# Optimization experiments

Hardware: AMD Instinct MI355X
Metric: run time of the kernel (lower is better)

Reference implementation:

```python
import jax, jax.numpy as jnp
import numpy as np

N = 50000   # nodes per graph stream
E = 800000  # edges per graph stream
G = 100     # graphs in batch
FIN, H = 74, 256


def setup_inputs() -> dict:
    key = jax.random.key(0)
    ks = jax.random.split(key, 16)
    d = {
        'xl': jax.random.normal(ks[0], (N, FIN), jnp.float32),
        'xr': jax.random.normal(ks[1], (N, FIN), jnp.float32),
        'src_l': jax.random.randint(ks[2], (E,), 0, N, jnp.int32),
        'dst_l': jax.random.randint(ks[3], (E,), 0, N, jnp.int32),
        'src_r': jax.random.randint(ks[4], (E,), 0, N, jnp.int32),
        'dst_r': jax.random.randint(ks[5], (E,), 0, N, jnp.int32),
        'gid_l': jnp.sort(jax.random.randint(ks[6], (N,), 0, G, jnp.int32)),
        'gid_r': jnp.sort(jax.random.randint(ks[7], (N,), 0, G, jnp.int32)),
        'W0': jax.random.normal(ks[8], (FIN, H), jnp.float32) / np.sqrt(FIN),
        'b0': jnp.zeros((H,), jnp.float32),
        'W1': jax.random.normal(ks[9], (H, H), jnp.float32) / np.sqrt(H),
        'b1': jnp.zeros((H,), jnp.float32),
        'W2': jax.random.normal(ks[10], (H, H), jnp.float32) / np.sqrt(H),
        'b2': jnp.zeros((H,), jnp.float32),
        'Wf1': jax.random.normal(ks[11], (2 * H, H), jnp.float32) / np.sqrt(2 * H),
        'bf1': jnp.zeros((H,), jnp.float32),
        'Wf2': jax.random.normal(ks[12], (H, 1), jnp.float32) / np.sqrt(H),
        'bf2': jnp.zeros((1,), jnp.float32),
    }
    return d


def _deg_isqrt(idx, n):
    deg = jax.ops.segment_sum(jnp.ones_like(idx, jnp.float32), idx, num_segments=n)
    return jax.lax.rsqrt(jnp.maximum(deg, 1.0))


def _graph_conv(x, src, dst, do_isq, di_isq, W, b):
    # DGL GraphConv, norm='both': h = relu(D_in^{-1/2} A D_out^{-1/2} X W + b)
    h = (x * do_isq[:, None]) @ W            # transform-first (in_feats >= out for layer0 path is fine mathematically)
    agg = jax.ops.segment_sum(h[src], dst, num_segments=x.shape[0])
    return jax.nn.relu(agg * di_isq[:, None] + b)


def reference(xl, xr, src_l, dst_l, src_r, dst_r, gid_l, gid_r,
              W0, b0, W1, b1, W2, b2, Wf1, bf1, Wf2, bf2):
    do_l, di_l = _deg_isqrt(src_l, N), _deg_isqrt(dst_l, N)
    do_r, di_r = _deg_isqrt(src_r, N), _deg_isqrt(dst_r, N)
    Ws, bs = (W0, W1, W2), (b0, b1, b2)
    hl, hr = xl, xr
    for W, b in zip(Ws, bs):  # shared weights across both graph streams
        hl = _graph_conv(hl, src_l, dst_l, do_l, di_l, W, b)
        hr = _graph_conv(hr, src_r, dst_r, do_r, di_r, W, b)
    pl = jax.ops.segment_sum(hl, gid_l, num_segments=G)  # dgl.sum_nodes
    pr = jax.ops.segment_sum(hr, gid_r, num_segments=G)
    z = jnp.concatenate([pl, pr], axis=-1)               # [G, 2H]
    return jax.nn.relu(z @ Wf1 + bf1) @ Wf2 + bf2        # [G, 1]
```

## Files before the change

### kernel.cpp

```cpp
#include <hip/hip_runtime.h>

#define N_NODES 50000
#define N_EDGES 800000
#define N_GRAPHS 100
#define FIN_DIM 74
#define X_LD 80
#define K0PAD 96
#define H_DIM 256
#define EG 3125
#define XSCALE_BLKS 15625
#define AGG_BLOCKS 25000
#define GEMM_BLKS 782
#define POOL_BLKS 782
#define SCAN_BLOCKS 196

typedef float f32x4 __attribute__((ext_vector_type(4)));
typedef unsigned short us2 __attribute__((ext_vector_type(2)));
typedef unsigned short us4 __attribute__((ext_vector_type(4)));
typedef unsigned short us8 __attribute__((ext_vector_type(8)));
typedef __bf16 bf16x8 __attribute__((ext_vector_type(8)));

__device__ __forceinline__ unsigned short f2bf(float x) {
    unsigned u = __builtin_bit_cast(unsigned, x);
    u += 0x7fff + ((u >> 16) & 1);
    return (unsigned short)(u >> 16);
}
__device__ __forceinline__ float bf2f(unsigned short h) {
    return __builtin_bit_cast(float, (unsigned)h << 16);
}


__device__ __forceinline__ void hist_body(int bid, const int* __restrict__ src,
                                          const int* __restrict__ dst,
                                          int* __restrict__ cs, int* __restrict__ fc,
                                          int* __restrict__ rk) {
    int e = bid * 256 + threadIdx.x;
    if (e < N_EDGES) {
        rk[e] = atomicAdd(&fc[dst[e]], 1);
        atomicAdd(&cs[src[e]], 1);
    }
}

__device__ __forceinline__ void scat_body(int bid, const int* __restrict__ src,
                                          const int* __restrict__ dst,
                                          const int* __restrict__ rp,
                                          const int* __restrict__ rk,
                                          int* __restrict__ col) {
    int e = bid * 256 + threadIdx.x;
    if (e < N_EDGES) {
        int d = dst[e];
        col[rp[d] + rk[e]] = src[e];
    }
}

__device__ __forceinline__ void xscale_body(int bid, const float* __restrict__ x,
                                            const float* __restrict__ dso,
                                            unsigned short* __restrict__ xp) {
    int id = bid * 256 + threadIdx.x;
    int n = id / X_LD, f = id - n * X_LD;
    float v = (f < FIN_DIM) ? x[(size_t)n * FIN_DIM + f] * dso[n] : 0.f;
    xp[id] = f2bf(v);
}

template<int LDI, int LDO>
__device__ __forceinline__ void agg_body(int nb, const unsigned short* __restrict__ h,
                                         const int* __restrict__ rp,
                                         const int* __restrict__ col,
                                         unsigned short* __restrict__ A) {
    int n = nb * 2 + (threadIdx.x >> 7);
    int f2 = (threadIdx.x & 127) * 2;
    if (f2 >= LDI) {
        if (f2 < LDO) { us2 z = {0, 0}; *(us2*)&A[(size_t)n * LDO + f2] = z; }
        return;
    }
    int beg = rp[n], end = rp[n + 1];
    float a0 = 0.f, a1 = 0.f, b0 = 0.f, b1 = 0.f;
    int j = beg;
    for (; j + 3 < end; j += 4) {
        int s0 = col[j], s1 = col[j + 1], s2 = col[j + 2], s3 = col[j + 3];
        us2 v0 = *(const us2*)&h[(size_t)s0 * LDI + f2];
        us2 v1 = *(const us2*)&h[(size_t)s1 * LDI + f2];
        us2 v2 = *(const us2*)&h[(size_t)s2 * LDI + f2];
        us2 v3 = *(const us2*)&h[(size_t)s3 * LDI + f2];
        a0 += bf2f(v0[0]) + bf2f(v1[0]);
        a1 += bf2f(v0[1]) + bf2f(v1[1]);
        b0 += bf2f(v2[0]) + bf2f(v3[0]);
        b1 += bf2f(v2[1]) + bf2f(v3[1]);
    }
    for (; j < end; ++j) {
        int s = col[j];
        us2 v = *(const us2*)&h[(size_t)s * LDI + f2];
        a0 += bf2f(v[0]);
        a1 += bf2f(v[1]);
    }
    us2 r = { f2bf(a0 + b0), f2bf(a1 + b1) };
    *(us2*)&A[(size_t)n * LDO + f2] = r;
}

__device__ __forceinline__ void pool_body(int nb, const unsigned short* __restrict__ h,
                                          const int* __restrict__ gid,
                                          float* __restrict__ pool) {
    int n0 = nb * 64;
    int f = threadIdx.x;
    int end = min(n0 + 64, N_NODES);
    float acc = 0.0f;
    int gcur = gid[n0];
    for (int i = n0; i < end; ++i) {
        int g = gid[i];
        if (g != gcur) {
            atomicAdd(&pool[(size_t)gcur * H_DIM + f], acc);
            acc = 0.0f;
            gcur = g;
        }
        acc += bf2f(h[(size_t)i * H_DIM + f]);
    }
    atomicAdd(&pool[(size_t)gcur * H_DIM + f], acc);
}

template<int K, int KW>
__device__ __forceinline__ void gemm_body(int id, const unsigned short* __restrict__ A,
                                          const float* __restrict__ W,
                                          const float* __restrict__ bias,
                                          const float* __restrict__ dsi,
                                          const float* __restrict__ scale,
                                          unsigned short* __restrict__ C,
                                          unsigned short* smem) {
    unsigned short (*Ah)[40] = (unsigned short(*)[40])smem;
    unsigned short (*Bh)[36] = (unsigned short(*)[36])(smem + 128 * 40);
    const int M = N_NODES;

    int tid = threadIdx.x;
    int lane = tid & 63, wid = tid >> 6;
    int wm = (wid >> 1) * 64, wn = (wid & 1) * 64;
    int bm = (id >> 1) * 128, bn = (id & 1) * 128;

    f32x4 acc[4][4] = {};
    int r0 = wm + (lane & 15);
    int c0 = wn + (lane & 15);
    int kA = (lane >> 4) * 8;

    for (int k0 = 0; k0 < K; k0 += 32) {
        #pragma unroll
        for (int i = 0; i < 2; ++i) {
            int q = tid + i * 256;
            int row = q >> 2, k8 = (q & 3) * 8;
            int gm = bm + row;
            us8 v = {0, 0, 0, 0, 0, 0, 0, 0};
            if (gm < M) v = *(const us8*)(A + (size_t)gm * K + k0 + k8);
            *(us8*)&Ah[row][k8] = v;
        }
        {
            int colx = tid & 127, kg = tid >> 7;
            #pragma unroll
            for (int g = 0; g < 4; ++g) {
                us4 hh;
                #pragma unroll
                for (int j = 0; j < 4; ++j) {
                    int gk = k0 + kg * 16 + g * 4 + j;
                    float w = (gk < KW) ? W[(size_t)gk * H_DIM + bn + colx] : 0.f;
                    hh[j] = f2bf(w);
                }
                *(us4*)&Bh[colx][kg * 16 + g * 4] = hh;
            }
        }
        __syncthreads();

        bf16x8 ah[4], bh[4];
        #pragma unroll
        for (int m = 0; m < 4; ++m)
            ah[m] = __builtin_bit_cast(bf16x8, *(const us8*)&Ah[r0 + m * 16][kA]);
        #pragma unroll
        for (int n = 0; n < 4; ++n) {
            us4 x0 = *(const us4*)&Bh[c0 + n * 16][kA];
            us4 x1 = *(const us4*)&Bh[c0 + n * 16][kA + 4];
            us8 x;
            x[0] = x0[0]; x[1] = x0[1]; x[2] = x0[2]; x[3] = x0[3];
            x[4] = x1[0]; x[5] = x1[1]; x[6] = x1[2]; x[7] = x1[3];
            bh[n] = __builtin_bit_cast(bf16x8, x);
        }

        #pragma unroll
        for (int m = 0; m < 4; ++m)
            #pragma unroll
            for (int n = 0; n < 4; ++n)
                acc[m][n] = __builtin_amdgcn_mfma_f32_16x16x32_bf16(ah[m], bh[n], acc[m][n], 0, 0, 0);
        __syncthreads();
    }

    int rowq = (lane >> 4) * 4;
    #pragma unroll
    for (int n = 0; n < 4; ++n) {
        int gn = bn + wn + n * 16 + (lane & 15);
        float bv = bias[gn];
        #pragma unroll
        for (int m = 0; m < 4; ++m) {
            #pragma unroll
            for (int j = 0; j < 4; ++j) {
                int gm = bm + wm + m * 16 + rowq + j;
                if (gm < M) {
                    float r = fmaxf(acc[m][n][j] * dsi[gm] + bv, 0.0f);
                    if (scale) r *= scale[gm];
                    C[(size_t)gm * H_DIM + gn] = f2bf(r);
                }
            }
        }
    }
}


__device__ __forceinline__ int block_excl_scan(int v, int* wsums) {
    int lane = threadIdx.x & 63, w = threadIdx.x >> 6;
    int x = v;
    #pragma unroll
    for (int ofs = 1; ofs < 64; ofs <<= 1) {
        int y = __shfl_up(x, ofs, 64);
        if (lane >= ofs) x += y;
    }
    if (lane == 63) wsums[w] = x;
    __syncthreads();
    int wo = 0;
    #pragma unroll
    for (int k = 0; k < 4; ++k) if (k < w) wo += wsums[k];
    return wo + x - v;
}

__global__ void hist_kernel(const int* __restrict__ src, const int* __restrict__ dst,
                            int* __restrict__ cs, int* __restrict__ fc, int* __restrict__ rk) {
    hist_body(blockIdx.x, src, dst, cs, fc, rk);
}

__global__ void deg_scan1_kernel(const int* __restrict__ cs, const int* __restrict__ fc,
                                 float* __restrict__ dso, float* __restrict__ dsi,
                                 int* __restrict__ rp, int* __restrict__ bs) {
    __shared__ int ws[4];
    int i = blockIdx.x * 256 + threadIdx.x;
    int v = 0;
    if (i < N_NODES) {
        dso[i] = rsqrtf(fmaxf((float)cs[i], 1.0f));
        v = fc[i];
        dsi[i] = rsqrtf(fmaxf((float)v, 1.0f));
    }
    int ex = block_excl_scan(v, ws);
    if (i < N_NODES) rp[i] = ex;
    if (threadIdx.x == 255) bs[blockIdx.x] = ex + v;
}

__global__ void scan2_kernel(int* __restrict__ bs, int nb) {
    __shared__ int ws[4];
    int i = threadIdx.x;
    int v = (i < nb) ? bs[i] : 0;
    int ex = block_excl_scan(v, ws);
    __syncthreads();
    if (i < nb) bs[i] = ex;
}

__global__ void scan3_kernel(int* __restrict__ rp, const int* __restrict__ bs) {
    int i = blockIdx.x * 256 + threadIdx.x;
    if (i < N_NODES) rp[i] += bs[blockIdx.x];
    if (i == 0) rp[N_NODES] = N_EDGES;
}

__global__ void fuse_hsx(const int* __restrict__ srcR, const int* __restrict__ dstR,
                         int* __restrict__ csR, int* __restrict__ fcR, int* __restrict__ rkR,
                         const int* __restrict__ srcL, const int* __restrict__ dstL,
                         const int* __restrict__ rpL, const int* __restrict__ rkL,
                         int* __restrict__ colL,
                         const float* __restrict__ xL, const float* __restrict__ dsoL,
                         unsigned short* __restrict__ xpL) {
    int bid = blockIdx.x;
    if (bid < EG)            hist_body(bid, srcR, dstR, csR, fcR, rkR);
    else if (bid < 2 * EG)   scat_body(bid - EG, srcL, dstL, rpL, rkL, colL);
    else                     xscale_body(bid - 2 * EG, xL, dsoL, xpL);
}

__global__ void fuse_dsagg0(const int* __restrict__ csR, const int* __restrict__ fcR,
                            float* __restrict__ dsoR, float* __restrict__ dsiR,
                            int* __restrict__ rpR, int* __restrict__ bsR,
                            const unsigned short* __restrict__ xpL, const int* __restrict__ rpL,
                            const int* __restrict__ colL, unsigned short* __restrict__ AL) {
    __shared__ int ws[4];
    int bid = blockIdx.x;
    if (bid < SCAN_BLOCKS) {
        int i = bid * 256 + threadIdx.x;
        int v = 0;
        if (i < N_NODES) {
            dsoR[i] = rsqrtf(fmaxf((float)csR[i], 1.0f));
            v = fcR[i];
            dsiR[i] = rsqrtf(fmaxf((float)v, 1.0f));
        }
        int ex = block_excl_scan(v, ws);
        if (i < N_NODES) rpR[i] = ex;
        if (threadIdx.x == 255) bsR[bid] = ex + v;
    } else {
        agg_body<X_LD, K0PAD>(bid - SCAN_BLOCKS, xpL, rpL, colL, AL);
    }
}

__global__ void fuse_sxagg(const int* __restrict__ srcR, const int* __restrict__ dstR,
                           const int* __restrict__ rpR, const int* __restrict__ rkR,
                           int* __restrict__ colR,
                           const float* __restrict__ xR, const float* __restrict__ dsoR,
                           unsigned short* __restrict__ xpR,
                           const unsigned short* __restrict__ hL, const int* __restrict__ rpL,
                           const int* __restrict__ colL, unsigned short* __restrict__ AL) {
    int bid = blockIdx.x;
    if (bid < EG)                      scat_body(bid, srcR, dstR, rpR, rkR, colR);
    else if (bid < EG + XSCALE_BLKS)   xscale_body(bid - EG, xR, dsoR, xpR);
    else                               agg_body<H_DIM, H_DIM>(bid - EG - XSCALE_BLKS, hL, rpL, colL, AL);
}

__global__ void fuse_agg_agg(const unsigned short* __restrict__ hL, const int* __restrict__ rpL,
                             const int* __restrict__ colL, unsigned short* __restrict__ AL,
                             const unsigned short* __restrict__ xpR, const int* __restrict__ rpR,
                             const int* __restrict__ colR, unsigned short* __restrict__ AR) {
    int bid = blockIdx.x;
    if (bid & 1) agg_body<X_LD, K0PAD>(bid >> 1, xpR, rpR, colR, AR);
    else         agg_body<H_DIM, H_DIM>(bid >> 1, hL, rpL, colL, AL);
}

__global__ void fuse_pool_agg(const unsigned short* __restrict__ hP, const int* __restrict__ gidP,
                              float* __restrict__ poolP,
                              const unsigned short* __restrict__ hA, const int* __restrict__ rpA,
                              const int* __restrict__ colA, unsigned short* __restrict__ outA) {
    int bid = blockIdx.x;
    if (bid < POOL_BLKS) pool_body(bid, hP, gidP, poolP);
    else                 agg_body<H_DIM, H_DIM>(bid - POOL_BLKS, hA, rpA, colA, outA);
}

template<int K, int KW>
__global__ __launch_bounds__(256) void gemm_kernel(
        const unsigned short* __restrict__ A, const float* __restrict__ W,
        const float* __restrict__ bias, const float* __restrict__ dsi,
        const float* __restrict__ scale, unsigned short* __restrict__ C) {
    __shared__ unsigned short smem[128 * 40 + 128 * 36];
    gemm_body<K, KW>(blockIdx.x, A, W, bias, dsi, scale, C, smem);
}

__global__ __launch_bounds__(256) void gemm_pair_kernel(
        const unsigned short* __restrict__ A1, const float* __restrict__ Wa,
        const float* __restrict__ ba, const float* __restrict__ dsi1, unsigned short* __restrict__ C1,
        const unsigned short* __restrict__ A2, const float* __restrict__ Wb,
        const float* __restrict__ bb, const float* __restrict__ dsi2,
        const float* __restrict__ sc2, unsigned short* __restrict__ C2) {
    __shared__ unsigned short smem[128 * 40 + 128 * 36];
    int bid = blockIdx.x;
    if (bid < GEMM_BLKS) gemm_body<H_DIM, H_DIM>(bid, A1, Wa, ba, dsi1, nullptr, C1, smem);
    else                 gemm_body<K0PAD, FIN_DIM>(bid - GEMM_BLKS, A2, Wb, bb, dsi2, sc2, C2, smem);
}

__global__ void agg_kernel(const unsigned short* __restrict__ h, const int* __restrict__ rp,
                           const int* __restrict__ col, unsigned short* __restrict__ A) {
    agg_body<H_DIM, H_DIM>(blockIdx.x, h, rp, col, A);
}

__global__ void pool_kernel(const unsigned short* __restrict__ h, const int* __restrict__ gid,
                            float* __restrict__ pool) {
    pool_body(blockIdx.x, h, gid, pool);
}

__global__ __launch_bounds__(256) void mlp_kernel(
        const float* __restrict__ pl, const float* __restrict__ pr,
        const float* __restrict__ Wf1, const float* __restrict__ bf1,
        const float* __restrict__ Wf2, const float* __restrict__ bf2,
        float* __restrict__ out) {
    __shared__ float z[512];
    __shared__ float red[256];
    int g = blockIdx.x, tid = threadIdx.x;
    z[tid] = pl[(size_t)g * H_DIM + tid];
    z[tid + 256] = pr[(size_t)g * H_DIM + tid];
    __syncthreads();
    float t = bf1[tid];
    #pragma unroll 8
    for (int k = 0; k < 512; ++k) t += z[k] * Wf1[(size_t)k * H_DIM + tid];
    t = fmaxf(t, 0.0f);
    red[tid] = t * Wf2[tid];
    __syncthreads();
    for (int ofs = 128; ofs > 0; ofs >>= 1) {
        if (tid < ofs) red[tid] += red[tid + ofs];
        __syncthreads();
    }
    if (tid == 0) out[g] = red[0] + bf2[0];
}


extern "C" void kernel_launch(void* const* d_in, const int* in_sizes, int n_in,
                              void* d_out, int out_size, void* d_ws, size_t ws_size,
                              hipStream_t stream) {
    const float* xl   = (const float*)d_in[0];
    const float* xr   = (const float*)d_in[1];
    const int* src_l  = (const int*)d_in[2];
    const int* dst_l  = (const int*)d_in[3];
    const int* src_r  = (const int*)d_in[4];
    const int* dst_r  = (const int*)d_in[5];
    const int* gid_l  = (const int*)d_in[6];
    const int* gid_r  = (const int*)d_in[7];
    const float* W0   = (const float*)d_in[8];
    const float* b0   = (const float*)d_in[9];
    const float* W1   = (const float*)d_in[10];
    const float* b1   = (const float*)d_in[11];
    const float* W2   = (const float*)d_in[12];
    const float* b2   = (const float*)d_in[13];
    const float* Wf1  = (const float*)d_in[14];
    const float* bf1  = (const float*)d_in[15];
    const float* Wf2  = (const float*)d_in[16];
    const float* bf2  = (const float*)d_in[17];
    float* out = (float*)d_out;
    (void)in_sizes; (void)n_in; (void)out_size; (void)ws_size;

    size_t off = 0;
    auto carve = [&](size_t bytes) {
        void* p = (char*)d_ws + off;
        off += (bytes + 255) & ~(size_t)255;
        return p;
    };
    const size_t NB4 = (size_t)N_NODES * 4;

    char* zstart = (char*)d_ws;
    int*   cs_l   = (int*)carve(NB4);
    int*   fc_l   = (int*)carve(NB4);
    int*   cs_r   = (int*)carve(NB4);
    int*   fc_r   = (int*)carve(NB4);
    float* pool_l = (float*)carve((size_t)N_GRAPHS * H_DIM * 4);
    float* pool_r = (float*)carve((size_t)N_GRAPHS * H_DIM * 4);
    size_t zbytes = off;

    float* dso_l = (float*)carve(NB4);
    float* dsi_l = (float*)carve(NB4);
    float* dso_r = (float*)carve(NB4);
    float* dsi_r = (float*)carve(NB4);
    int*   rp_l  = (int*)carve((size_t)(N_NODES + 1) * 4);
    int*   rp_r  = (int*)carve((size_t)(N_NODES + 1) * 4);
    int*   col_l = (int*)carve((size_t)N_EDGES * 4);
    int*   col_r = (int*)carve((size_t)N_EDGES * 4);
    int*   rk_l  = (int*)carve((size_t)N_EDGES * 4);
    int*   rk_r  = (int*)carve((size_t)N_EDGES * 4);
    int*   bs_l  = (int*)carve((size_t)SCAN_BLOCKS * 4);
    int*   bs_r  = (int*)carve((size_t)SCAN_BLOCKS * 4);

    unsigned short* xp_l  = (unsigned short*)carve((size_t)N_NODES * X_LD * 2);
    unsigned short* xp_r  = (unsigned short*)carve((size_t)N_NODES * X_LD * 2);
    unsigned short* bufA_l = (unsigned short*)carve((size_t)N_NODES * H_DIM * 2);
    unsigned short* bufA_r = (unsigned short*)carve((size_t)N_NODES * H_DIM * 2);
    unsigned short* bufH_l = (unsigned short*)carve((size_t)N_NODES * H_DIM * 2);
    unsigned short* bufH_r = (unsigned short*)carve((size_t)N_NODES * H_DIM * 2);

    hipMemsetAsync(zstart, 0, zbytes, stream);

    hist_kernel<<<EG, 256, 0, stream>>>(src_l, dst_l, cs_l, fc_l, rk_l);
    deg_scan1_kernel<<<SCAN_BLOCKS, 256, 0, stream>>>(cs_l, fc_l, dso_l, dsi_l, rp_l, bs_l);
    scan2_kernel<<<1, 256, 0, stream>>>(bs_l, SCAN_BLOCKS);
    scan3_kernel<<<SCAN_BLOCKS, 256, 0, stream>>>(rp_l, bs_l);

    fuse_hsx<<<2 * EG + XSCALE_BLKS, 256, 0, stream>>>(
        src_r, dst_r, cs_r, fc_r, rk_r,
        src_l, dst_l, rp_l, rk_l, col_l,
        xl, dso_l, xp_l);

    fuse_dsagg0<<<SCAN_BLOCKS + AGG_BLOCKS, 256, 0, stream>>>(
        cs_r, fc_r, dso_r, dsi_r, rp_r, bs_r,
        xp_l, rp_l, col_l, bufA_l);
    scan2_kernel<<<1, 256, 0, stream>>>(bs_r, SCAN_BLOCKS);
    scan3_kernel<<<SCAN_BLOCKS, 256, 0, stream>>>(rp_r, bs_r);

    gemm_kernel<K0PAD, FIN_DIM><<<GEMM_BLKS, 256, 0, stream>>>(bufA_l, W0, b0, dsi_l, dso_l, bufH_l);

    fuse_sxagg<<<EG + XSCALE_BLKS + AGG_BLOCKS, 256, 0, stream>>>(
        src_r, dst_r, rp_r, rk_r, col_r,
        xr, dso_r, xp_r,
        bufH_l, rp_l, col_l, bufA_l);

    gemm_kernel<H_DIM, H_DIM><<<GEMM_BLKS, 256, 0, stream>>>(bufA_l, W1, b1, dsi_l, dso_l, bufH_l);

    fuse_agg_agg<<<2 * AGG_BLOCKS, 256, 0, stream>>>(
        bufH_l, rp_l, col_l, bufA_l,
        xp_r, rp_r, col_r, bufA_r);

    gemm_pair_kernel<<<2 * GEMM_BLKS, 256, 0, stream>>>(
        bufA_l, W2, b2, dsi_l, bufH_l,
        bufA_r, W0, b0, dsi_r, dso_r, bufH_r);

    fuse_pool_agg<<<POOL_BLKS + AGG_BLOCKS, 256, 0, stream>>>(
        bufH_l, gid_l, pool_l,
        bufH_r, rp_r, col_r, bufA_r);

    gemm_kernel<H_DIM, H_DIM><<<GEMM_BLKS, 256, 0, stream>>>(bufA_r, W1, b1, dsi_r, dso_r, bufH_r);

    agg_kernel<<<AGG_BLOCKS, 256, 0, stream>>>(bufH_r, rp_r, col_r, bufA_r);
    gemm_kernel<H_DIM, H_DIM><<<GEMM_BLKS, 256, 0, stream>>>(bufA_r, W2, b2, dsi_r, nullptr, bufH_r);
    pool_kernel<<<POOL_BLKS, 256, 0, stream>>>(bufH_r, gid_r, pool_r);

    mlp_kernel<<<N_GRAPHS, 256, 0, stream>>>(pool_l, pool_r, Wf1, bf1, Wf2, bf2, out);
}
```

Before: 921.3 us.

## Slice node features into column panels and pre-convert weights to bf16

```diff
diff --git a/kernel.cpp b/kernel.cpp
--- a/kernel.cpp
+++ b/kernel.cpp
@@ -4,19 +4,19 @@
 #define N_EDGES 800000
 #define N_GRAPHS 100
 #define FIN_DIM 74
-#define X_LD 80
-#define K0PAD 96
+#define K0 96
 #define H_DIM 256
 #define EG 3125
-#define XSCALE_BLKS 15625
-#define AGG_BLOCKS 25000
+#define XS_BLKS 18750
+#define WCONV_BLKS 608
+#define AGG0_BLKS 3128
+#define AGGH_BLKS 6256
 #define GEMM_BLKS 782
 #define POOL_BLKS 782
 #define SCAN_BLOCKS 196
 
 typedef float f32x4 __attribute__((ext_vector_type(4)));
-typedef unsigned short us2 __attribute__((ext_vector_type(2)));
-typedef unsigned short us4 __attribute__((ext_vector_type(4)));
+typedef unsigned int u32x4 __attribute__((ext_vector_type(4)));
 typedef unsigned short us8 __attribute__((ext_vector_type(8)));
 typedef __bf16 bf16x8 __attribute__((ext_vector_type(8)));
 
@@ -27,6 +27,14 @@
 }
 __device__ __forceinline__ float bf2f(unsigned short h) {
     return __builtin_bit_cast(float, (unsigned)h << 16);
+}
+__device__ __forceinline__ void acc8(float* a, us8 v) {
+    u32x4 w = __builtin_bit_cast(u32x4, v);
+    #pragma unroll
+    for (int i = 0; i < 4; ++i) {
+        a[2 * i]     += __builtin_bit_cast(float, w[i] << 16);
+        a[2 * i + 1] += __builtin_bit_cast(float, w[i] & 0xffff0000u);
+    }
 }
 
 
@@ -57,44 +65,63 @@
                                             const float* __restrict__ dso,
                                             unsigned short* __restrict__ xp) {
     int id = bid * 256 + threadIdx.x;
-    int n = id / X_LD, f = id - n * X_LD;
+    int n = id / 96, f = id - n * 96;
     float v = (f < FIN_DIM) ? x[(size_t)n * FIN_DIM + f] * dso[n] : 0.f;
-    xp[id] = f2bf(v);
-}
-
-template<int LDI, int LDO>
-__device__ __forceinline__ void agg_body(int nb, const unsigned short* __restrict__ h,
+    xp[(size_t)(f >> 4) * (N_NODES * 16) + (size_t)n * 16 + (f & 15)] = f2bf(v);
+}
+
+__device__ __forceinline__ void wconv_body(int bid, const float* __restrict__ W0,
+                                           const float* __restrict__ W1,
+                                           const float* __restrict__ W2,
+                                           unsigned short* __restrict__ Wt) {
+    int id = bid * 256 + threadIdx.x;
+    if (id < 256 * 96) {
+        int n = id / 96, k = id - n * 96;
+        float v = (k < FIN_DIM) ? W0[(size_t)k * H_DIM + n] : 0.f;
+        Wt[id] = f2bf(v);
+    } else if (id < 256 * 96 + 65536) {
+        int id2 = id - 256 * 96;
+        int n = id2 >> 8, k = id2 & 255;
+        Wt[id] = f2bf(W1[(size_t)k * H_DIM + n]);
+    } else {
+        int id3 = id - 256 * 96 - 65536;
+        int n = id3 >> 8, k = id3 & 255;
+        Wt[id] = f2bf(W2[(size_t)k * H_DIM + n]);
+    }
+}
+
+template<int SW, int NACT, int NSL>
+__device__ __forceinline__ void agg_body(int abid, int cg,
+                                         const unsigned short* __restrict__ h,
                                          const int* __restrict__ rp,
                                          const int* __restrict__ col,
                                          unsigned short* __restrict__ A) {
-    int n = nb * 2 + (threadIdx.x >> 7);
-    int f2 = (threadIdx.x & 127) * 2;
-    if (f2 >= LDI) {
-        if (f2 < LDO) { us2 z = {0, 0}; *(us2*)&A[(size_t)n * LDO + f2] = z; }
-        return;
-    }
+    const int CPB = SW / 8;
+    const int NPB = 256 / CPB;
+    if (cg >= NSL) return;
+    int slot = threadIdx.x & (CPB - 1);
+    int n = (abid >> 3) * NPB + threadIdx.x / CPB;
+    if (n >= N_NODES) return;
+    unsigned short* dst = A + (size_t)cg * (N_NODES * SW) + (size_t)n * SW + slot * 8;
+    if (cg >= NACT) { us8 z = {}; *(us8*)dst = z; return; }
+    const unsigned short* hs = h + (size_t)cg * (N_NODES * SW) + slot * 8;
     int beg = rp[n], end = rp[n + 1];
-    float a0 = 0.f, a1 = 0.f, b0 = 0.f, b1 = 0.f;
+    float a[8] = {};
     int j = beg;
     for (; j + 3 < end; j += 4) {
         int s0 = col[j], s1 = col[j + 1], s2 = col[j + 2], s3 = col[j + 3];
-        us2 v0 = *(const us2*)&h[(size_t)s0 * LDI + f2];
-        us2 v1 = *(const us2*)&h[(size_t)s1 * LDI + f2];
-        us2 v2 = *(const us2*)&h[(size_t)s2 * LDI + f2];
-        us2 v3 = *(const us2*)&h[(size_t)s3 * LDI + f2];
-        a0 += bf2f(v0[0]) + bf2f(v1[0]);
-        a1 += bf2f(v0[1]) + bf2f(v1[1]);
-        b0 += bf2f(v2[0]) + bf2f(v3[0]);
-        b1 += bf2f(v2[1]) + bf2f(v3[1]);
-    }
-    for (; j < end; ++j) {
-        int s = col[j];
-        us2 v = *(const us2*)&h[(size_t)s * LDI + f2];
-        a0 += bf2f(v[0]);
-        a1 += bf2f(v[1]);
-    }
-    us2 r = { f2bf(a0 + b0), f2bf(a1 + b1) };
-    *(us2*)&A[(size_t)n * LDO + f2] = r;
+        us8 v0 = *(const us8*)(hs + (size_t)s0 * SW);
+        us8 v1 = *(const us8*)(hs + (size_t)s1 * SW);
+        us8 v2 = *(const us8*)(hs + (size_t)s2 * SW);
+        us8 v3 = *(const us8*)(hs + (size_t)s3 * SW);
+        acc8(a, v0); acc8(a, v1); acc8(a, v2); acc8(a, v3);
+    }
+    for (; j < end; ++j)
+        acc8(a, *(const us8*)(hs + (size_t)col[j] * SW));
+    us8 r;
+    #pragma unroll
+    for (int i = 0; i < 8; ++i) r[i] = f2bf(a[i]);
+    *(us8*)dst = r;
 }
 
 __device__ __forceinline__ void pool_body(int nb, const unsigned short* __restrict__ h,
@@ -102,6 +129,7 @@
                                           float* __restrict__ pool) {
     int n0 = nb * 64;
     int f = threadIdx.x;
+    const unsigned short* hf = h + (size_t)(f >> 5) * (N_NODES * 32) + (f & 31);
     int end = min(n0 + 64, N_NODES);
     float acc = 0.0f;
     int gcur = gid[n0];
@@ -112,21 +140,21 @@
             acc = 0.0f;
             gcur = g;
         }
-        acc += bf2f(h[(size_t)i * H_DIM + f]);
+        acc += bf2f(hf[(size_t)i * 32]);
     }
     atomicAdd(&pool[(size_t)gcur * H_DIM + f], acc);
 }
 
-template<int K, int KW>
+template<int K, int SW>
 __device__ __forceinline__ void gemm_body(int id, const unsigned short* __restrict__ A,
-                                          const float* __restrict__ W,
+                                          const unsigned short* __restrict__ Wt,
                                           const float* __restrict__ bias,
                                           const float* __restrict__ dsi,
                                           const float* __restrict__ scale,
                                           unsigned short* __restrict__ C,
                                           unsigned short* smem) {
     unsigned short (*Ah)[40] = (unsigned short(*)[40])smem;
-    unsigned short (*Bh)[36] = (unsigned short(*)[36])(smem + 128 * 40);
+    unsigned short (*Bh)[40] = (unsigned short(*)[40])(smem + 128 * 40);
     const int M = N_NODES;
 
     int tid = threadIdx.x;
@@ -145,23 +173,20 @@
             int q = tid + i * 256;
             int row = q >> 2, k8 = (q & 3) * 8;
             int gm = bm + row;
-            us8 v = {0, 0, 0, 0, 0, 0, 0, 0};
-            if (gm < M) v = *(const us8*)(A + (size_t)gm * K + k0 + k8);
+            int kk = k0 + k8;
+            us8 v = {};
+            if (gm < M)
+                v = *(const us8*)(A + (size_t)(kk / SW) * ((size_t)N_NODES * SW)
+                                    + (size_t)gm * SW + (kk % SW));
             *(us8*)&Ah[row][k8] = v;
         }
         {
             int colx = tid & 127, kg = tid >> 7;
-            #pragma unroll
-            for (int g = 0; g < 4; ++g) {
-                us4 hh;
-                #pragma unroll
-                for (int j = 0; j < 4; ++j) {
-                    int gk = k0 + kg * 16 + g * 4 + j;
-                    float w = (gk < KW) ? W[(size_t)gk * H_DIM + bn + colx] : 0.f;
-                    hh[j] = f2bf(w);
-                }
-                *(us4*)&Bh[colx][kg * 16 + g * 4] = hh;
-            }
+            const unsigned short* wsrc = Wt + (size_t)(bn + colx) * K + k0 + kg * 16;
+            us8 w0 = *(const us8*)(wsrc);
+            us8 w1 = *(const us8*)(wsrc + 8);
+            *(us8*)&Bh[colx][kg * 16] = w0;
+            *(us8*)&Bh[colx][kg * 16 + 8] = w1;
         }
         __syncthreads();
 
@@ -170,14 +195,8 @@
         for (int m = 0; m < 4; ++m)
             ah[m] = __builtin_bit_cast(bf16x8, *(const us8*)&Ah[r0 + m * 16][kA]);
         #pragma unroll
-        for (int n = 0; n < 4; ++n) {
-            us4 x0 = *(const us4*)&Bh[c0 + n * 16][kA];
-            us4 x1 = *(const us4*)&Bh[c0 + n * 16][kA + 4];
-            us8 x;
-            x[0] = x0[0]; x[1] = x0[1]; x[2] = x0[2]; x[3] = x0[3];
-            x[4] = x1[0]; x[5] = x1[1]; x[6] = x1[2]; x[7] = x1[3];
-            bh[n] = __builtin_bit_cast(bf16x8, x);
-        }
+        for (int n = 0; n < 4; ++n)
+            bh[n] = __builtin_bit_cast(bf16x8, *(const us8*)&Bh[c0 + n * 16][kA]);
 
         #pragma unroll
         for (int m = 0; m < 4; ++m)
@@ -192,6 +211,7 @@
     for (int n = 0; n < 4; ++n) {
         int gn = bn + wn + n * 16 + (lane & 15);
         float bv = bias[gn];
+        unsigned short* cs = C + (size_t)(gn >> 5) * (N_NODES * 32) + (gn & 31);
         #pragma unroll
         for (int m = 0; m < 4; ++m) {
             #pragma unroll
@@ -200,7 +220,7 @@
                 if (gm < M) {
                     float r = fmaxf(acc[m][n][j] * dsi[gm] + bv, 0.0f);
                     if (scale) r *= scale[gm];
-                    C[(size_t)gm * H_DIM + gn] = f2bf(r);
+                    cs[(size_t)gm * 32] = f2bf(r);
                 }
             }
         }
@@ -224,9 +244,13 @@
     return wo + x - v;
 }
 
-__global__ void hist_kernel(const int* __restrict__ src, const int* __restrict__ dst,
-                            int* __restrict__ cs, int* __restrict__ fc, int* __restrict__ rk) {
-    hist_body(blockIdx.x, src, dst, cs, fc, rk);
+__global__ void k_whist(const float* __restrict__ W0, const float* __restrict__ W1,
+                        const float* __restrict__ W2, unsigned short* __restrict__ Wt,
+                        const int* __restrict__ src, const int* __restrict__ dst,
+                        int* __restrict__ cs, int* __restrict__ fc, int* __restrict__ rk) {
+    int bid = blockIdx.x;
+    if (bid < WCONV_BLKS) wconv_body(bid, W0, W1, W2, Wt);
+    else                  hist_body(bid - WCONV_BLKS, src, dst, cs, fc, rk);
 }
 
 __global__ void deg_scan1_kernel(const int* __restrict__ cs, const int* __restrict__ fc,
@@ -292,7 +316,7 @@
         if (i < N_NODES) rpR[i] = ex;
         if (threadIdx.x == 255) bsR[bid] = ex + v;
     } else {
-        agg_body<X_LD, K0PAD>(bid - SCAN_BLOCKS, xpL, rpL, colL, AL);
+        agg_body<16, 5, 6>(bid - SCAN_BLOCKS, blockIdx.x & 7, xpL, rpL, colL, AL);
     }
 }
 
@@ -304,9 +328,9 @@
                            const unsigned short* __restrict__ hL, const int* __restrict__ rpL,
                            const int* __restrict__ colL, unsigned short* __restrict__ AL) {
     int bid = blockIdx.x;
-    if (bid < EG)                      scat_body(bid, srcR, dstR, rpR, rkR, colR);
-    else if (bid < EG + XSCALE_BLKS)   xscale_body(bid - EG, xR, dsoR, xpR);
-    else                               agg_body<H_DIM, H_DIM>(bid - EG - XSCALE_BLKS, hL, rpL, colL, AL);
+    if (bid < EG)                    scat_body(bid, srcR, dstR, rpR, rkR, colR);
+    else if (bid < EG + XS_BLKS)     xscale_body(bid - EG, xR, dsoR, xpR);
+    else agg_body<32, 8, 8>(bid - EG - XS_BLKS, blockIdx.x & 7, hL, rpL, colL, AL);
 }
 
 __global__ void fuse_agg_agg(const unsigned short* __restrict__ hL, const int* __restrict__ rpL,
@@ -314,8 +338,8 @@
                              const unsigned short* __restrict__ xpR, const int* __restrict__ rpR,
                              const int* __restrict__ colR, unsigned short* __restrict__ AR) {
     int bid = blockIdx.x;
-    if (bid & 1) agg_body<X_LD, K0PAD>(bid >> 1, xpR, rpR, colR, AR);
-    else         agg_body<H_DIM, H_DIM>(bid >> 1, hL, rpL, colL, AL);
+    if (bid < AGGH_BLKS) agg_body<32, 8, 8>(bid, blockIdx.x & 7, hL, rpL, colL, AL);
+    else agg_body<16, 5, 6>(bid - AGGH_BLKS, blockIdx.x & 7, xpR, rpR, colR, AR);
 }
 
 __global__ void fuse_pool_agg(const unsigned short* __restrict__ hP, const int* __restrict__ gidP,
@@ -324,33 +348,33 @@
                               const int* __restrict__ colA, unsigned short* __restrict__ outA) {
     int bid = blockIdx.x;
     if (bid < POOL_BLKS) pool_body(bid, hP, gidP, poolP);
-    else                 agg_body<H_DIM, H_DIM>(bid - POOL_BLKS, hA, rpA, colA, outA);
-}
-
-template<int K, int KW>
+    else agg_body<32, 8, 8>(bid - POOL_BLKS, blockIdx.x & 7, hA, rpA, colA, outA);
+}
+
+template<int K, int SW>
 __global__ __launch_bounds__(256) void gemm_kernel(
-        const unsigned short* __restrict__ A, const float* __restrict__ W,
+        const unsigned short* __restrict__ A, const unsigned short* __restrict__ Wt,
         const float* __restrict__ bias, const float* __restrict__ dsi,
         const float* __restrict__ scale, unsigned short* __restrict__ C) {
-    __shared__ unsigned short smem[128 * 40 + 128 * 36];
-    gemm_body<K, KW>(blockIdx.x, A, W, bias, dsi, scale, C, smem);
+    __shared__ unsigned short smem[2 * 128 * 40];
+    gemm_body<K, SW>(blockIdx.x, A, Wt, bias, dsi, scale, C, smem);
 }
 
 __global__ __launch_bounds__(256) void gemm_pair_kernel(
-        const unsigned short* __restrict__ A1, const float* __restrict__ Wa,
-        const float* __restrict__ ba, const float* __restrict__ dsi1, unsigned short* __restrict__ C1,
-        const unsigned short* __restrict__ A2, const float* __restrict__ Wb,
-        const float* __restrict__ bb, const float* __restrict__ dsi2,
+        const unsigned short* __restrict__ A1, const unsigned short* __restrict__ Wt2,
+        const float* __restrict__ b2_, const float* __restrict__ dsi1, unsigned short* __restrict__ C1,
+        const unsigned short* __restrict__ A2, const unsigned short* __restrict__ Wt0,
+        const float* __restrict__ b0_, const float* __restrict__ dsi2,
         const float* __restrict__ sc2, unsigned short* __restrict__ C2) {
-    __shared__ unsigned short smem[128 * 40 + 128 * 36];
-    int bid = blockIdx.x;
-    if (bid < GEMM_BLKS) gemm_body<H_DIM, H_DIM>(bid, A1, Wa, ba, dsi1, nullptr, C1, smem);
-    else                 gemm_body<K0PAD, FIN_DIM>(bid - GEMM_BLKS, A2, Wb, bb, dsi2, sc2, C2, smem);
+    __shared__ unsigned short smem[2 * 128 * 40];
+    int bid = blockIdx.x;
+    if (bid < GEMM_BLKS) gemm_body<H_DIM, 32>(bid, A1, Wt2, b2_, dsi1, nullptr, C1, smem);
+    else                 gemm_body<K0, 16>(bid - GEMM_BLKS, A2, Wt0, b0_, dsi2, sc2, C2, smem);
 }
 
 __global__ void agg_kernel(const unsigned short* __restrict__ h, const int* __restrict__ rp,
                            const int* __restrict__ col, unsigned short* __restrict__ A) {
-    agg_body<H_DIM, H_DIM>(blockIdx.x, h, rp, col, A);
+    agg_body<32, 8, 8>(blockIdx.x, blockIdx.x & 7, h, rp, col, A);
 }
 
 __global__ void pool_kernel(const unsigned short* __restrict__ h, const int* __restrict__ gid,
@@ -437,8 +461,12 @@
     int*   bs_l  = (int*)carve((size_t)SCAN_BLOCKS * 4);
     int*   bs_r  = (int*)carve((size_t)SCAN_BLOCKS * 4);
 
-    unsigned short* xp_l  = (unsigned short*)carve((size_t)N_NODES * X_LD * 2);
-    unsigned short* xp_r  = (unsigned short*)carve((size_t)N_NODES * X_LD * 2);
+    unsigned short* Wt    = (unsigned short*)carve((size_t)(256 * 96 + 2 * 65536) * 2);
+    unsigned short* Wt0   = Wt;
+    unsigned short* Wt1   = Wt + 256 * 96;
+    unsigned short* Wt2   = Wt + 256 * 96 + 65536;
+    unsigned short* xp_l  = (unsigned short*)carve((size_t)N_NODES * 96 * 2);
+    unsigned short* xp_r  = (unsigned short*)carve((size_t)N_NODES * 96 * 2);
     unsigned short* bufA_l = (unsigned short*)carve((size_t)N_NODES * H_DIM * 2);
     unsigned short* bufA_r = (unsigned short*)carve((size_t)N_NODES * H_DIM * 2);
     unsigned short* bufH_l = (unsigned short*)carve((size_t)N_NODES * H_DIM * 2);
@@ -446,47 +474,48 @@
 
     hipMemsetAsync(zstart, 0, zbytes, stream);
 
-    hist_kernel<<<EG, 256, 0, stream>>>(src_l, dst_l, cs_l, fc_l, rk_l);
+    k_whist<<<WCONV_BLKS + EG, 256, 0, stream>>>(W0, W1, W2, Wt,
+                                                 src_l, dst_l, cs_l, fc_l, rk_l);
     deg_scan1_kernel<<<SCAN_BLOCKS, 256, 0, stream>>>(cs_l, fc_l, dso_l, dsi_l, rp_l, bs_l);
     scan2_kernel<<<1, 256, 0, stream>>>(bs_l, SCAN_BLOCKS);
     scan3_kernel<<<SCAN_BLOCKS, 256, 0, stream>>>(rp_l, bs_l);
 
-    fuse_hsx<<<2 * EG + XSCALE_BLKS, 256, 0, stream>>>(
+    fuse_hsx<<<2 * EG + XS_BLKS, 256, 0, stream>>>(
         src_r, dst_r, cs_r, fc_r, rk_r,
         src_l, dst_l, rp_l, rk_l, col_l,
         xl, dso_l, xp_l);
 
-    fuse_dsagg0<<<SCAN_BLOCKS + AGG_BLOCKS, 256, 0, stream>>>(
+    fuse_dsagg0<<<SCAN_BLOCKS + AGG0_BLKS, 256, 0, stream>>>(
         cs_r, fc_r, dso_r, dsi_r, rp_r, bs_r,
         xp_l, rp_l, col_l, bufA_l);
     scan2_kernel<<<1, 256, 0, stream>>>(bs_r, SCAN_BLOCKS);
     scan3_kernel<<<SCAN_BLOCKS, 256, 0, stream>>>(rp_r, bs_r);
 
-    gemm_kernel<K0PAD, FIN_DIM><<<GEMM_BLKS, 256, 0, stream>>>(bufA_l, W0, b0, dsi_l, dso_l, bufH_l);
-
-    fuse_sxagg<<<EG + XSCALE_BLKS + AGG_BLOCKS, 256, 0, stream>>>(
+    gemm_kernel<K0, 16><<<GEMM_BLKS, 256, 0, stream>>>(bufA_l, Wt0, b0, dsi_l, dso_l, bufH_l);
+
+    fuse_sxagg<<<EG + XS_BLKS + AGGH_BLKS, 256, 0, stream>>>(
         src_r, dst_r, rp_r, rk_r, col_r,
         xr, dso_r, xp_r,
         bufH_l, rp_l, col_l, bufA_l);
 
-    gemm_kernel<H_DIM, H_DIM><<<GEMM_BLKS, 256, 0, stream>>>(bufA_l, W1, b1, dsi_l, dso_l, bufH_l);
-
-    fuse_agg_agg<<<2 * AGG_BLOCKS, 256, 0, stream>>>(
+    gemm_kernel<H_DIM, 32><<<GEMM_BLKS, 256, 0, stream>>>(bufA_l, Wt1, b1, dsi_l, dso_l, bufH_l);
+
+    fuse_agg_agg<<<AGGH_BLKS + AGG0_BLKS, 256, 0, stream>>>(
         bufH_l, rp_l, col_l, bufA_l,
         xp_r, rp_r, col_r, bufA_r);
 
     gemm_pair_kernel<<<2 * GEMM_BLKS, 256, 0, stream>>>(
-        bufA_l, W2, b2, dsi_l, bufH_l,
-        bufA_r, W0, b0, dsi_r, dso_r, bufH_r);
-
-    fuse_pool_agg<<<POOL_BLKS + AGG_BLOCKS, 256, 0, stream>>>(
+        bufA_l, Wt2, b2, dsi_l, bufH_l,
+        bufA_r, Wt0, b0, dsi_r, dso_r, bufH_r);
+
+    fuse_pool_agg<<<POOL_BLKS + AGGH_BLKS, 256, 0, stream>>>(
         bufH_l, gid_l, pool_l,
         bufH_r, rp_r, col_r, bufA_r);
 
-    gemm_kernel<H_DIM, H_DIM><<<GEMM_BLKS, 256, 0, stream>>>(bufA_r, W1, b1, dsi_r, dso_r, bufH_r);
-
-    agg_kernel<<<AGG_BLOCKS, 256, 0, stream>>>(bufH_r, rp_r, col_r, bufA_r);
-    gemm_kernel<H_DIM, H_DIM><<<GEMM_BLKS, 256, 0, stream>>>(bufA_r, W2, b2, dsi_r, nullptr, bufH_r);
+    gemm_kernel<H_DIM, 32><<<GEMM_BLKS, 256, 0, stream>>>(bufA_r, Wt1, b1, dsi_r, dso_r, bufH_r);
+
+    agg_kernel<<<AGGH_BLKS, 256, 0, stream>>>(bufH_r, rp_r, col_r, bufA_r);
+    gemm_kernel<H_DIM, 32><<<GEMM_BLKS, 256, 0, stream>>>(bufA_r, Wt2, b2, dsi_r, nullptr, bufH_r);
     pool_kernel<<<POOL_BLKS, 256, 0, stream>>>(bufH_r, gid_r, pool_r);
 
     mlp_kernel<<<N_GRAPHS, 256, 0, stream>>>(pool_l, pool_r, Wf1, bf1, Wf2, bf2, out);
```

New measurement: 757.2 us. 17.8% less time.
